# Kernel tuning notes

Measured on AMD Instinct MI355X. Metric: run time of the kernel, lower is better.

## Reference

```python
import jax, jax.numpy as jnp
import numpy as np

# Gemma-2B style config
B, S, HID = 2, 2048, 2048
H, KH, D = 8, 1, 256          # query heads, kv heads, head_dim
THETA = 10000.0


def setup_inputs() -> dict:
    key = jax.random.key(0)
    ks = jax.random.split(key, 6)
    s = 0.02  # init scale for weights
    return {
        "hidden_states": jax.random.normal(ks[0], (B, S, HID), dtype=jnp.float32),
        "attention_mask": jnp.zeros((B, S), dtype=jnp.float32),  # additive mask over kv axis
        "position_ids": jnp.broadcast_to(jnp.arange(S, dtype=jnp.int32), (B, S)),
        "Wq": jax.random.normal(ks[1], (H * D, HID), dtype=jnp.float32) * s,
        "bq": jnp.zeros((H * D,), dtype=jnp.float32),
        "Wk": jax.random.normal(ks[2], (KH * D, HID), dtype=jnp.float32) * s,
        "bk": jnp.zeros((KH * D,), dtype=jnp.float32),
        "Wv": jax.random.normal(ks[3], (KH * D, HID), dtype=jnp.float32) * s,
        "bv": jnp.zeros((KH * D,), dtype=jnp.float32),
        "Wo": jax.random.normal(ks[4], (HID, H * D), dtype=jnp.float32) * s,
        "bo": jnp.zeros((HID,), dtype=jnp.float32),
    }


def _rope(x, position_ids):
    # x: [b, s, h, d]; rotate-half RoPE per head, computed in fp32 as in the module.
    half = D // 2
    inv_freq = 1.0 / (THETA ** (jnp.arange(0, D, 2, dtype=jnp.float32) / D))  # [d/2]
    freqs = position_ids.astype(jnp.float32)[:, :, None] * inv_freq            # [b, s, d/2]
    cos = jnp.cos(freqs)[:, :, None, :]  # [b, s, 1, d/2]
    sin = jnp.sin(freqs)[:, :, None, :]
    x1, x2 = x[..., :half], x[..., half:]
    return jnp.concatenate([cos * x1 - sin * x2, sin * x1 + cos * x2], axis=-1).astype(x.dtype)


def reference(hidden_states, attention_mask, position_ids, Wq, bq, Wk, bk, Wv, bv, Wo, bo):
    b, s, _ = hidden_states.shape
    q = (hidden_states @ Wq.T + bq).reshape(b, s, H, D)
    k = (hidden_states @ Wk.T + bk).reshape(b, s, KH, D)
    v = (hidden_states @ Wv.T + bv).reshape(b, s, KH, D)
    q = _rope(q, position_ids)
    k = _rope(k, position_ids)
    # GQA: broadcast the KV heads across query-head groups
    groups = H // KH
    k = jnp.repeat(k, groups, axis=2)  # [b, s, H, D]
    v = jnp.repeat(v, groups, axis=2)
    scores = jnp.einsum('bnhd,bmhd->bhnm', q, k) * (D ** -0.5)  # [b, H, s, s]
    scores = scores + attention_mask[:, None, None, :]
    attn = jax.nn.softmax(scores, axis=-1)  # dropout p=0.0 -> identity
    out = jnp.einsum('bhnm,bmhd->bnhd', attn, v).reshape(b, s, H * D)
    out = out @ Wo.T + bo
    return (out, attn)
```

## Files before the change

### kernel.cpp

```cpp
#include <hip/hip_runtime.h>

#define B_ 2
#define S_ 2048
#define HID_ 2048
#define H_ 8
#define D_ 256
#define NQKV 2560

typedef unsigned short u16;
typedef __attribute__((ext_vector_type(8))) short bf16x8;
typedef __attribute__((ext_vector_type(4))) float f32x4;

__device__ __forceinline__ u16 f2b(float x) {
    unsigned u = __float_as_uint(x);
    unsigned rb = (u >> 16) & 1u;
    u += 0x7fffu + rb;
    return (u16)(u >> 16);
}

__device__ __forceinline__ void load_lds16(const u16* g, u16* l) {
    __builtin_amdgcn_global_load_lds(
        (const __attribute__((address_space(1))) void*)g,
        (__attribute__((address_space(3))) void*)l, 16, 0, 0);
}

__global__ __launch_bounds__(256) void cvt_bf16(const float* __restrict__ in,
                                                u16* __restrict__ out, int n) {
    int i = (blockIdx.x * 256 + threadIdx.x) * 4;
    if (i >= n) return;
    float4 f = *(const float4*)(in + i);
    union { u16 u[4]; uint2 v; } pk;
    pk.u[0] = f2b(f.x); pk.u[1] = f2b(f.y); pk.u[2] = f2b(f.z); pk.u[3] = f2b(f.w);
    *(uint2*)(out + i) = pk.v;
}

__global__ __launch_bounds__(256) void concat_bias(const float* __restrict__ bq,
                                                   const float* __restrict__ bk,
                                                   const float* __restrict__ bv,
                                                   float* __restrict__ dst) {
    int i = blockIdx.x * 256 + threadIdx.x;
    if (i >= NQKV) return;
    float v;
    if (i < H_ * D_) v = bq[i];
    else if (i < H_ * D_ + D_) v = bk[i - H_ * D_];
    else v = bv[i - H_ * D_ - D_];
    dst[i] = v;
}

__global__ __launch_bounds__(256) void rope_kernel(const float* __restrict__ x,
                                                   int rowStride, int colOff,
                                                   const int* __restrict__ pos_ids,
                                                   u16* __restrict__ out, int nHeads) {
    int idx = blockIdx.x * 256 + threadIdx.x;
    int d   = idx & 127;
    int tmp = idx >> 7;
    int h   = tmp % nHeads;
    int n   = tmp / nHeads;
    int pos = pos_ids[n];
    float ang = (float)pos * expf(-(float)d * (9.210340371976184f / 128.0f));
    float s, c;
    sincosf(ang, &s, &c);
    size_t src = (size_t)n * rowStride + colOff + (size_t)h * D_;
    float x1 = x[src + d], x2 = x[src + d + 128];
    size_t dst = ((size_t)n * nHeads + h) * D_;
    out[dst + d]       = f2b(c * x1 - s * x2);
    out[dst + d + 128] = f2b(s * x1 + c * x2);
}

__global__ __launch_bounds__(256) void transpose_v(const float* __restrict__ v,
                                                   int rowStride, int colOff,
                                                   u16* __restrict__ vT) {
    __shared__ float t[32][33];
    int b = blockIdx.z;
    int s0 = blockIdx.x * 32, d0 = blockIdx.y * 32;
    int tx = threadIdx.x, ty = threadIdx.y;
#pragma unroll
    for (int i = 0; i < 4; ++i)
        t[ty + i * 8][tx] = v[((size_t)b * S_ + s0 + ty + i * 8) * rowStride + colOff + d0 + tx];
    __syncthreads();
#pragma unroll
    for (int i = 0; i < 4; ++i)
        vT[(size_t)b * D_ * S_ + (size_t)(d0 + ty + i * 8) * S_ + s0 + tx] = f2b(t[tx][ty + i * 8]);
}

__global__ __launch_bounds__(256, 2) void score_softmax(
    const u16* __restrict__ q_b, const u16* __restrict__ k_b,
    const float* __restrict__ mask, float* __restrict__ attn,
    u16* __restrict__ attn_b) {
    __shared__ __align__(16) u16 qs[16 * 256];
    __shared__ __align__(16) u16 ks[2][64 * 256];
    __shared__ float redm[4][16], reds[4][16];

    const int z = blockIdx.z;
    const int bb = z >> 3, hh = z & 7;
    const int n0 = blockIdx.x * 16;
    const int tid = threadIdx.x;
    const int lane = tid & 63, wave = tid >> 6;
    const int l15 = lane & 15, quad = lane >> 4;

    const int tr5 = tid >> 5;
    const int gsw = ((tid & 31) ^ tr5) * 8;
    const size_t koff = (size_t)tr5 * D_ + gsw;

    const u16* qsrc  = q_b + (((size_t)bb * S_ + n0) * H_ + hh) * D_;
    const u16* kbase = k_b + (size_t)bb * S_ * D_;

#pragma unroll
    for (int i = 0; i < 2; ++i)
        load_lds16(qsrc + (size_t)(i * 8 + tr5) * (H_ * D_) + gsw,
                   qs + (size_t)(i * 256 + wave * 64) * 8);

#pragma unroll
    for (int j = 0; j < 8; ++j)
        load_lds16(kbase + (size_t)(j * 8) * D_ + koff,
                   ks[0] + (size_t)(j * 256 + wave * 64) * 8);

    f32x4 acc[32];
#pragma unroll
    for (int ct = 0; ct < 32; ++ct)
#pragma unroll
        for (int r = 0; r < 4; ++r) acc[ct][r] = 0.f;

    __syncthreads();

    bf16x8 av[8];
#pragma unroll
    for (int kk = 0; kk < 8; ++kk)
        av[kk] = *(const bf16x8*)&qs[l15 * 256 + (((kk * 4 + quad) ^ (l15 & 7)) * 8)];

    const int rb = wave * 16 + l15;
    const int rbo = rb * 256;

#pragma unroll
    for (int t = 0; t < 32; ++t) {
        if (t < 31) {
            u16* dst = ks[(t + 1) & 1];
            const u16* src = kbase + (size_t)((t + 1) * 64) * D_ + koff;
#pragma unroll
            for (int j = 0; j < 8; ++j)
                load_lds16(src + (size_t)(j * 8) * D_,
                           dst + (size_t)(j * 256 + wave * 64) * 8);
        }
        const u16* kst = ks[t & 1];
        bf16x8 bv[8];
#pragma unroll
        for (int kk = 0; kk < 8; ++kk)
            bv[kk] = *(const bf16x8*)&kst[rbo + (((kk * 4 + quad) ^ (rb & 7)) * 8)];
#pragma unroll
        for (int kk = 0; kk < 8; ++kk)
            acc[t] = __builtin_amdgcn_mfma_f32_16x16x32_bf16(av[kk], bv[kk], acc[t], 0, 0, 0);
        __syncthreads();
    }

    const float sc = 0.0625f;
    const float* maskb = mask + (size_t)bb * S_ + wave * 16 + l15;
    float mx[4] = {-3.4e38f, -3.4e38f, -3.4e38f, -3.4e38f};
#pragma unroll
    for (int ct = 0; ct < 32; ++ct) {
        float mkv = maskb[ct * 64];
#pragma unroll
        for (int r = 0; r < 4; ++r) {
            float xv = acc[ct][r] * sc + mkv;
            acc[ct][r] = xv;
            mx[r] = fmaxf(mx[r], xv);
        }
    }
#pragma unroll
    for (int off = 1; off < 16; off <<= 1)
#pragma unroll
        for (int r = 0; r < 4; ++r) mx[r] = fmaxf(mx[r], __shfl_xor(mx[r], off));
    if (l15 == 0) {
#pragma unroll
        for (int r = 0; r < 4; ++r) redm[wave][quad * 4 + r] = mx[r];
    }
    __syncthreads();
    const float LOG2E = 1.4426950408889634f;
    float fm[4], sm[4];
#pragma unroll
    for (int r = 0; r < 4; ++r) {
        int rw = quad * 4 + r;
        fm[r] = fmaxf(fmaxf(redm[0][rw], redm[1][rw]),
                      fmaxf(redm[2][rw], redm[3][rw]));
        sm[r] = 0.f;
    }
#pragma unroll
    for (int ct = 0; ct < 32; ++ct)
#pragma unroll
        for (int r = 0; r < 4; ++r) {
            float e = exp2f((acc[ct][r] - fm[r]) * LOG2E);
            acc[ct][r] = e;
            sm[r] += e;
        }
#pragma unroll
    for (int off = 1; off < 16; off <<= 1)
#pragma unroll
        for (int r = 0; r < 4; ++r) sm[r] += __shfl_xor(sm[r], off);
    if (l15 == 0) {
#pragma unroll
        for (int r = 0; r < 4; ++r) reds[wave][quad * 4 + r] = sm[r];
    }
    __syncthreads();

    size_t obase = ((size_t)(bb * H_ + hh) * S_ + n0 + quad * 4) * S_
                 + wave * 16 + l15;
#pragma unroll
    for (int r = 0; r < 4; ++r) {
        int rw = quad * 4 + r;
        float inv = 1.f / (reds[0][rw] + reds[1][rw] + reds[2][rw] + reds[3][rw]);
        float* ao = attn + obase + (size_t)r * S_;
#pragma unroll
        for (int ct = 0; ct < 32; ++ct) {
            float p = acc[ct][r] * inv;
            ao[ct * 64] = p;
            acc[ct][r] = p;
        }
    }
    if (attn_b) {
        u16* ab = attn_b + obase;
#pragma unroll
        for (int r = 0; r < 4; ++r) {
            u16* abr = ab + (size_t)r * S_;
#pragma unroll
            for (int ct = 0; ct < 32; ++ct) abr[ct * 64] = f2b(acc[ct][r]);
        }
    }
}

#define TILE_M 128
#define TILE_N 128
#define TILE_K 32

template <bool C_IS_BF16>
__global__ __launch_bounds__(256, 2) void gemm_async(
    const u16* __restrict__ Ap, const u16* __restrict__ Bp, void* __restrict__ Cp,
    const float* __restrict__ bias, int lda, int ldb, int ldc, int K,
    long sAb, long sAh, long sBb, long sBh, long sCb, long sCh, int numH) {
    __shared__ __align__(16) u16 As[TILE_M * TILE_K];
    __shared__ __align__(16) u16 Bs[TILE_N * TILE_K];

    int z = blockIdx.z;
    int bb = z / numH, hh = z % numH;
    const u16* Ab = Ap + (long)bb * sAb + (long)hh * sAh;
    const u16* Bb = Bp + (long)bb * sBb + (long)hh * sBh;
    long cOff = (long)bb * sCb + (long)hh * sCh;

    const int m0 = blockIdx.y * TILE_M;
    const int n0 = blockIdx.x * TILE_N;
    const int tid = threadIdx.x;
    const int lane = tid & 63, wave = tid >> 6;
    const int l15 = lane & 15, quad = lane >> 4;
    const int waveM = wave >> 1, waveN = wave & 1;

    f32x4 acc[4][4];
#pragma unroll
    for (int mt = 0; mt < 4; ++mt)
#pragma unroll
        for (int nt = 0; nt < 4; ++nt)
#pragma unroll
            for (int r = 0; r < 4; ++r) acc[mt][nt][r] = 0.f;

    int rowS[2], colS[2];
    u16 *lA[2], *lB[2];
#pragma unroll
    for (int i = 0; i < 2; ++i) {
        int c = i * 256 + tid;
        rowS[i] = c >> 2;
        colS[i] = (((c & 3) ^ ((rowS[i] >> 1) & 3)) * 8);
        lA[i] = As + (size_t)(i * 256 + wave * 64) * 8;
        lB[i] = Bs + (size_t)(i * 256 + wave * 64) * 8;
    }

    for (int k0 = 0; k0 < K; k0 += TILE_K) {
#pragma unroll
        for (int i = 0; i < 2; ++i) {
            load_lds16(Ab + (size_t)(m0 + rowS[i]) * lda + k0 + colS[i], lA[i]);
            load_lds16(Bb + (size_t)(n0 + rowS[i]) * ldb + k0 + colS[i], lB[i]);
        }
        __syncthreads();

        bf16x8 av[4], bv[4];
#pragma unroll
        for (int t = 0; t < 4; ++t) {
            int ra = waveM * 64 + t * 16 + l15;
            av[t] = *(bf16x8*)&As[ra * TILE_K + ((quad ^ ((ra >> 1) & 3)) * 8)];
            int rb = waveN * 64 + t * 16 + l15;
            bv[t] = *(bf16x8*)&Bs[rb * TILE_K + ((quad ^ ((rb >> 1) & 3)) * 8)];
        }
#pragma unroll
        for (int mt = 0; mt < 4; ++mt)
#pragma unroll
            for (int nt = 0; nt < 4; ++nt)
                acc[mt][nt] = __builtin_amdgcn_mfma_f32_16x16x32_bf16(av[mt], bv[nt],
                                                                      acc[mt][nt], 0, 0, 0);
        __syncthreads();
    }

#pragma unroll
    for (int mt = 0; mt < 4; ++mt) {
        int row = m0 + waveM * 64 + mt * 16 + quad * 4;
#pragma unroll
        for (int nt = 0; nt < 4; ++nt) {
            int col = n0 + waveN * 64 + nt * 16 + l15;
            float bia = bias ? bias[col] : 0.f;
#pragma unroll
            for (int r = 0; r < 4; ++r) {
                float val = acc[mt][nt][r] + bia;
                if constexpr (C_IS_BF16)
                    ((u16*)Cp)[cOff + (size_t)(row + r) * ldc + col] = f2b(val);
                else
                    ((float*)Cp)[cOff + (size_t)(row + r) * ldc + col] = val;
            }
        }
    }
}

#define LDSK 40
__global__ __launch_bounds__(256, 2) void gemm_slow_f32a(
    const float* __restrict__ Ap, const u16* __restrict__ Bp, u16* __restrict__ Cp,
    int lda, int ldb, int ldc, int K,
    long sAb, long sAh, long sBb, long sBh, long sCb, long sCh, int numH) {
    __shared__ __align__(16) u16 As[TILE_M * LDSK];
    __shared__ __align__(16) u16 Bs[TILE_N * LDSK];
    int z = blockIdx.z;
    int bb = z / numH, hh = z % numH;
    const float* Af = Ap + (long)bb * sAb + (long)hh * sAh;
    const u16* Bb = Bp + (long)bb * sBb + (long)hh * sBh;
    long cOff = (long)bb * sCb + (long)hh * sCh;
    const int m0 = blockIdx.y * TILE_M, n0 = blockIdx.x * TILE_N;
    const int tid = threadIdx.x;
    const int lane = tid & 63, wave = tid >> 6;
    const int l15 = lane & 15, quad = lane >> 4;
    const int waveM = wave >> 1, waveN = wave & 1;
    f32x4 acc[4][4];
#pragma unroll
    for (int mt = 0; mt < 4; ++mt)
#pragma unroll
        for (int nt = 0; nt < 4; ++nt)
#pragma unroll
            for (int r = 0; r < 4; ++r) acc[mt][nt][r] = 0.f;
    for (int k0 = 0; k0 < K; k0 += TILE_K) {
#pragma unroll
        for (int i = 0; i < 2; ++i) {
            int c = tid + i * 256;
            int row = c >> 2, col = (c & 3) * 8;
            const float* src = Af + (size_t)(m0 + row) * lda + k0 + col;
            float4 f0 = *(const float4*)src;
            float4 f1 = *(const float4*)(src + 4);
            union { u16 u[8]; uint4 v; } pk;
            pk.u[0] = f2b(f0.x); pk.u[1] = f2b(f0.y); pk.u[2] = f2b(f0.z); pk.u[3] = f2b(f0.w);
            pk.u[4] = f2b(f1.x); pk.u[5] = f2b(f1.y); pk.u[6] = f2b(f1.z); pk.u[7] = f2b(f1.w);
            *(uint4*)&As[row * LDSK + col] = pk.v;
            *(uint4*)&Bs[row * LDSK + col] =
                *(const uint4*)(Bb + (size_t)(n0 + row) * ldb + k0 + col);
        }
        __syncthreads();
        bf16x8 av[4], bv[4];
#pragma unroll
        for (int t = 0; t < 4; ++t) {
            av[t] = *(bf16x8*)&As[(waveM * 64 + t * 16 + l15) * LDSK + quad * 8];
            bv[t] = *(bf16x8*)&Bs[(waveN * 64 + t * 16 + l15) * LDSK + quad * 8];
        }
#pragma unroll
        for (int mt = 0; mt < 4; ++mt)
#pragma unroll
            for (int nt = 0; nt < 4; ++nt)
                acc[mt][nt] = __builtin_amdgcn_mfma_f32_16x16x32_bf16(av[mt], bv[nt],
                                                                      acc[mt][nt], 0, 0, 0);
        __syncthreads();
    }
#pragma unroll
    for (int mt = 0; mt < 4; ++mt) {
        int row = m0 + waveM * 64 + mt * 16 + quad * 4;
#pragma unroll
        for (int nt = 0; nt < 4; ++nt) {
            int col = n0 + waveN * 64 + nt * 16 + l15;
#pragma unroll
            for (int r = 0; r < 4; ++r)
                Cp[cOff + (size_t)(row + r) * ldc + col] = f2b(acc[mt][nt][r]);
        }
    }
}

extern "C" void kernel_launch(void* const* d_in, const int* in_sizes, int n_in,
                              void* d_out, int out_size, void* d_ws, size_t ws_size,
                              hipStream_t stream) {
    const float* hs   = (const float*)d_in[0];
    const float* mask = (const float*)d_in[1];
    const int*   pos  = (const int*)d_in[2];
    const float* Wq = (const float*)d_in[3];
    const float* bq = (const float*)d_in[4];
    const float* Wk = (const float*)d_in[5];
    const float* bk = (const float*)d_in[6];
    const float* Wv = (const float*)d_in[7];
    const float* bv = (const float*)d_in[8];
    const float* Wo = (const float*)d_in[9];
    const float* bo = (const float*)d_in[10];

    float* out  = (float*)d_out;
    float* attn = (float*)d_out + (size_t)B_ * S_ * HID_;

    char* ws = (char*)d_ws;
    size_t need = 0;
    u16* hs_b    = (u16*)(ws);          need += (size_t)B_ * S_ * HID_ * 2;
    u16* Wqkv_b  = (u16*)(ws + need);   need += (size_t)NQKV * HID_ * 2;
    u16* Wo_b    = (u16*)(ws + need);   need += (size_t)HID_ * H_ * D_ * 2;
    float* qkv_f = (float*)(ws + need); need += (size_t)B_ * S_ * NQKV * 4;
    u16* q_b     = (u16*)(ws + need);   need += (size_t)B_ * S_ * H_ * D_ * 2;
    u16* k_b     = (u16*)(ws + need);   need += (size_t)B_ * S_ * D_ * 2;
    u16* vT_b    = (u16*)(ws + need);   need += (size_t)B_ * D_ * S_ * 2;
    float* bqkv  = (float*)(ws + need); need += (size_t)NQKV * 4 + 4096;
    need &= ~(size_t)255;
    u16* attn_b  = (u16*)(ws + need);
    size_t need_big = need + (size_t)B_ * H_ * S_ * S_ * 2;
    bool big = ws_size >= need_big;
    u16* ctx_b = hs_b;

    cvt_bf16<<<dim3((B_ * S_ * HID_) / 1024), 256, 0, stream>>>(hs, hs_b, B_ * S_ * HID_);
    cvt_bf16<<<dim3((H_ * D_ * HID_) / 1024), 256, 0, stream>>>(Wq, Wqkv_b, H_ * D_ * HID_);
    cvt_bf16<<<dim3((D_ * HID_) / 1024), 256, 0, stream>>>(Wk, Wqkv_b + (size_t)H_ * D_ * HID_, D_ * HID_);
    cvt_bf16<<<dim3((D_ * HID_) / 1024), 256, 0, stream>>>(Wv, Wqkv_b + (size_t)(H_ * D_ + D_) * HID_, D_ * HID_);
    cvt_bf16<<<dim3((HID_ * H_ * D_) / 1024), 256, 0, stream>>>(Wo, Wo_b, HID_ * H_ * D_);
    concat_bias<<<dim3((NQKV + 255) / 256), 256, 0, stream>>>(bq, bk, bv, bqkv);

    gemm_async<false><<<dim3(NQKV / TILE_N, (B_ * S_) / TILE_M, 1), 256, 0, stream>>>(
        hs_b, Wqkv_b, qkv_f, bqkv, HID_, HID_, NQKV, HID_,
        0, 0, 0, 0, 0, 0, 1);

    rope_kernel<<<dim3((B_ * S_ * H_ * 128) / 256), 256, 0, stream>>>(
        qkv_f, NQKV, 0, pos, q_b, H_);
    rope_kernel<<<dim3((B_ * S_ * 1 * 128) / 256), 256, 0, stream>>>(
        qkv_f, NQKV, H_ * D_, pos, k_b, 1);
    transpose_v<<<dim3(S_ / 32, D_ / 32, B_), dim3(32, 8), 0, stream>>>(
        qkv_f, NQKV, H_ * D_ + D_, vT_b);

    score_softmax<<<dim3(S_ / 16, 1, B_ * H_), 256, 0, stream>>>(
        q_b, k_b, mask, attn, big ? attn_b : nullptr);

    if (big) {
        gemm_async<true><<<dim3(D_ / TILE_N, S_ / TILE_M, B_ * H_), 256, 0, stream>>>(
            attn_b, vT_b, ctx_b, nullptr, S_, S_, H_ * D_, S_,
            (long)H_ * S_ * S_, (long)S_ * S_,
            (long)D_ * S_, 0,
            (long)S_ * H_ * D_, D_,
            H_);
    } else {
        gemm_slow_f32a<<<dim3(D_ / TILE_N, S_ / TILE_M, B_ * H_), 256, 0, stream>>>(
            attn, vT_b, ctx_b, S_, S_, H_ * D_, S_,
            (long)H_ * S_ * S_, (long)S_ * S_,
            (long)D_ * S_, 0,
            (long)S_ * H_ * D_, D_,
            H_);
    }

    gemm_async<false><<<dim3(HID_ / TILE_N, (B_ * S_) / TILE_M, 1), 256, 0, stream>>>(
        ctx_b, Wo_b, out, bo, H_ * D_, H_ * D_, HID_, H_ * D_,
        0, 0, 0, 0, 0, 0, 1);
}
```

Measured before the change: 719.7 us.

## Load Q/K fragments directly from global into registers in score kernel

Drops the LDS staging of the Q tile and the double-buffered K tiles in the score/softmax kernel. Each lane now reads its MFMA operand fragments straight from global memory, with two register buffers used to prefetch the next K tile. This removes the LDS traffic and the per-iteration block barrier. In exchange, global traffic is less coalesced (32-byte pieces per lane with a 512-byte row stride), each wave fetches K independently through cache, and register pressure rises.

```diff
diff --git a/kernel.cpp b/kernel.cpp
--- a/kernel.cpp
+++ b/kernel.cpp
@@ -87,8 +87,6 @@
     const u16* __restrict__ q_b, const u16* __restrict__ k_b,
     const float* __restrict__ mask, float* __restrict__ attn,
     u16* __restrict__ attn_b) {
-    __shared__ __align__(16) u16 qs[16 * 256];
-    __shared__ __align__(16) u16 ks[2][64 * 256];
     __shared__ float redm[4][16], reds[4][16];
 
     const int z = blockIdx.z;
@@ -98,22 +96,13 @@
     const int lane = tid & 63, wave = tid >> 6;
     const int l15 = lane & 15, quad = lane >> 4;
 
-    const int tr5 = tid >> 5;
-    const int gsw = ((tid & 31) ^ tr5) * 8;
-    const size_t koff = (size_t)tr5 * D_ + gsw;
-
-    const u16* qsrc  = q_b + (((size_t)bb * S_ + n0) * H_ + hh) * D_;
-    const u16* kbase = k_b + (size_t)bb * S_ * D_;
-
-#pragma unroll
-    for (int i = 0; i < 2; ++i)
-        load_lds16(qsrc + (size_t)(i * 8 + tr5) * (H_ * D_) + gsw,
-                   qs + (size_t)(i * 256 + wave * 64) * 8);
-
-#pragma unroll
-    for (int j = 0; j < 8; ++j)
-        load_lds16(kbase + (size_t)(j * 8) * D_ + koff,
-                   ks[0] + (size_t)(j * 256 + wave * 64) * 8);
+    const u16* qrow = q_b + (((size_t)bb * S_ + n0 + l15) * H_ + hh) * D_ + quad * 8;
+    const u16* krow = k_b + ((size_t)bb * S_ + wave * 16 + l15) * D_ + quad * 8;
+
+    bf16x8 av[8];
+#pragma unroll
+    for (int kk = 0; kk < 8; ++kk)
+        av[kk] = *(const bf16x8*)(qrow + kk * 32);
 
     f32x4 acc[32];
 #pragma unroll
@@ -121,35 +110,32 @@
 #pragma unroll
         for (int r = 0; r < 4; ++r) acc[ct][r] = 0.f;
 
-    __syncthreads();
-
-    bf16x8 av[8];
+    bf16x8 bvA[8], bvB[8];
 #pragma unroll
     for (int kk = 0; kk < 8; ++kk)
-        av[kk] = *(const bf16x8*)&qs[l15 * 256 + (((kk * 4 + quad) ^ (l15 & 7)) * 8)];
-
-    const int rb = wave * 16 + l15;
-    const int rbo = rb * 256;
+        bvA[kk] = *(const bf16x8*)(krow + kk * 32);
 
 #pragma unroll
     for (int t = 0; t < 32; ++t) {
         if (t < 31) {
-            u16* dst = ks[(t + 1) & 1];
-            const u16* src = kbase + (size_t)((t + 1) * 64) * D_ + koff;
-#pragma unroll
-            for (int j = 0; j < 8; ++j)
-                load_lds16(src + (size_t)(j * 8) * D_,
-                           dst + (size_t)(j * 256 + wave * 64) * 8);
-        }
-        const u16* kst = ks[t & 1];
-        bf16x8 bv[8];
-#pragma unroll
-        for (int kk = 0; kk < 8; ++kk)
-            bv[kk] = *(const bf16x8*)&kst[rbo + (((kk * 4 + quad) ^ (rb & 7)) * 8)];
-#pragma unroll
-        for (int kk = 0; kk < 8; ++kk)
-            acc[t] = __builtin_amdgcn_mfma_f32_16x16x32_bf16(av[kk], bv[kk], acc[t], 0, 0, 0);
-        __syncthreads();
+            const u16* src = krow + (size_t)(t + 1) * 64 * D_;
+            if (t & 1) {
+#pragma unroll
+                for (int kk = 0; kk < 8; ++kk) bvA[kk] = *(const bf16x8*)(src + kk * 32);
+            } else {
+#pragma unroll
+                for (int kk = 0; kk < 8; ++kk) bvB[kk] = *(const bf16x8*)(src + kk * 32);
+            }
+        }
+        if (t & 1) {
+#pragma unroll
+            for (int kk = 0; kk < 8; ++kk)
+                acc[t] = __builtin_amdgcn_mfma_f32_16x16x32_bf16(av[kk], bvB[kk], acc[t], 0, 0, 0);
+        } else {
+#pragma unroll
+            for (int kk = 0; kk < 8; ++kk)
+                acc[t] = __builtin_amdgcn_mfma_f32_16x16x32_bf16(av[kk], bvA[kk], acc[t], 0, 0, 0);
+        }
     }
 
     const float sc = 0.0625f;
```

After: 884.7 us. 22.9% more time.
